# Optimization experiments

Hardware: AMD Instinct MI355X
Metric: run time of the kernel (lower is better)

## Reference

```python
import jax, jax.numpy as jnp
import numpy as np

N = 12288   # nodes
E = 393216  # edges (avg degree 32)
B = 16      # graphs in batch
F_IN = 15   # node feature dim
H = 32      # hidden_dim
EMB = 64    # embedding_dim
NC = 11     # num_classes
EDIM = 2    # edge feature dim
EPS = 1e-5  # BatchNorm eps


def _bn(x, gamma, beta):
    # training-mode BatchNorm1d: biased batch variance, matches torch normalization
    mu = jnp.mean(x, axis=0)
    var = jnp.var(x, axis=0)
    return gamma * (x - mu) * jax.lax.rsqrt(var + EPS) + beta


def setup_inputs() -> dict:
    key = jax.random.key(0)
    ks = jax.random.split(key, 16)
    def p(k, shape, s=0.05):
        return jax.random.normal(k, shape, dtype=jnp.float32) * s
    z = lambda *s: jnp.zeros(s, jnp.float32)
    o = lambda *s: jnp.ones(s, jnp.float32)
    return {
        "x": jax.random.normal(ks[0], (N, F_IN), dtype=jnp.float32),
        "edge_attr": jax.random.normal(ks[1], (E, EDIM), dtype=jnp.float32),
        "w_edge": p(ks[2], (EDIM, 1)), "b_edge": z(1),
        "w1": p(ks[3], (F_IN, H)), "b1": z(H), "g1": o(H), "be1": z(H),
        "w2": p(ks[4], (H, 2 * H)), "b2": z(2 * H), "g2": o(2 * H), "be2": z(2 * H),
        "w3": p(ks[5], (2 * H, EMB)), "b3": z(EMB), "g3": o(EMB), "be3": z(EMB),
        "wf1": p(ks[6], (EMB, 512)), "bf1": z(512), "gf1": o(512), "bef1": z(512),
        "wf2": p(ks[7], (512, 256)), "bf2": z(256), "gf2": o(256), "bef2": z(256),
        "wf3": p(ks[8], (256, NC)), "bf3": z(NC),
        "edge_index": jax.random.randint(ks[9], (2, E), 0, N, dtype=jnp.int64)
                      if jax.config.jax_enable_x64 else jax.random.randint(ks[9], (2, E), 0, N),
        "batch": jnp.sort(jax.random.randint(ks[10], (N,), 0, B)),
    }


def reference(x, edge_attr, w_edge, b_edge,
              w1, b1, g1, be1, w2, b2, g2, be2, w3, b3, g3, be3,
              wf1, bf1, gf1, bef1, wf2, bf2, gf2, bef2, wf3, bf3,
              edge_index, batch):
    # edge weights: sigmoid(Linear(edge_attr)) -> [E]
    ew = jax.nn.sigmoid(edge_attr @ w_edge + b_edge)[:, 0]
    # dense adjacency with self loops, accumulate duplicates (sparse_coo.to_dense)
    loop = jnp.arange(N)
    row = jnp.concatenate([edge_index[0], loop])
    col = jnp.concatenate([edge_index[1], loop])
    w_aug = jnp.concatenate([ew, jnp.ones((N,), ew.dtype)])
    adj = jnp.zeros((N, N), ew.dtype).at[row, col].add(w_aug)
    # symmetric degree normalization D^-1/2 A D^-1/2
    deg = adj.sum(axis=1)
    dis = jnp.where(deg > 0, jax.lax.rsqrt(jnp.where(deg > 0, deg, 1.0)), 0.0)
    support = dis[:, None] * adj * dis[None, :]
    # three GCN layers: support @ x @ W + b, BN, relu
    h = jax.nn.relu(_bn(support @ x @ w1 + b1, g1, be1))
    h = jax.nn.relu(_bn(support @ h @ w2 + b2, g2, be2))
    h = jax.nn.relu(_bn(support @ h @ w3 + b3, g3, be3))
    # global max pool per graph (empty graphs -> zeros)
    seg = jax.ops.segment_max(h, batch, num_segments=B)
    cnt = jax.ops.segment_sum(jnp.ones((N,), h.dtype), batch, num_segments=B)
    emb = jnp.where(cnt[:, None] > 0, seg, 0.0)
    # MLP head (dropout = identity at inference)
    o = jax.nn.relu(_bn(emb @ wf1 + bf1, gf1, bef1))
    o = jax.nn.relu(_bn(o @ wf2 + bf2, gf2, bef2))
    logits = o @ wf3 + bf3
    return jax.nn.log_softmax(logits, axis=1), emb
```

## Files before the change

### kernel.cpp

```cpp
#include <hip/hip_runtime.h>
#include <hip/hip_bf16.h>

#define NN   12288
#define EE   393216
#define WELL 128
#define NELL (NN*WELL)
#define BG   16
#define FIN  15
#define FH1  32
#define FH2  64
#define NCL  11
#define BNEPS 1e-5f
#define NBANK 32

typedef unsigned long long u64;
static inline int cdiv(long a, long b){ return (int)((a + b - 1) / b); }

__device__ __forceinline__ int getIdx(const void* p, long i, int is64){
  return is64 ? (int)((const long long*)p)[i] : ((const int*)p)[i];
}

__device__ __forceinline__ float degOf(u64 dc){
  return 1.0f + (float)(unsigned)(dc & 0xffffffffull) * (1.0f/1048576.0f);
}

__global__ void k_pre(u64* deg_cnt, float* csp1, float* csp2, float* csp3,
                      float* embf, const void* ei, const void* batch, int* flags){
  int g = blockIdx.x*256 + threadIdx.x;
  if (g < NN) deg_cnt[g] = 0ull;
  if (g < NBANK*128){ csp1[g] = 0.f; csp2[g] = 0.f; csp3[g] = 0.f; }
  if (g < BG*64) embf[g] = 0.f;
  if (blockIdx.x == 0 && threadIdx.x < 64){
    const int* a = (const int*)ei;
    unsigned long long m0 = __ballot(a[2*threadIdx.x + 1] == 0);
    const int* b = (const int*)batch;
    int j = 96*threadIdx.x;
    unsigned long long m1 = __ballot(b[2*j + 1] == 0);
    if (threadIdx.x == 0){
      flags[0] = (m0 == ~0ull) ? 1 : 0;
      flags[1] = (m1 == ~0ull) ? 1 : 0;
    }
  }
}

__global__ void k_edge(const float* ea, const float* we, const float* bedg,
                       const void* ei, const int* flags, u64* deg_cnt, u64* csr_p){
  int e = blockIdx.x*256 + threadIdx.x;
  if (e >= EE) return;
  int is64 = flags[0];
  float2 eav = ((const float2*)ea)[e];
  float z = eav.x*we[0] + eav.y*we[1] + bedg[0];
  float w = 1.0f/(1.0f + expf(-z));
  int r = getIdx(ei, e, is64);
  int c = getIdx(ei, (long)EE + e, is64);
  u64 add = (1ull << 32) | (u64)__float2uint_rn(w * 1048576.0f);
  u64 old = atomicAdd(&deg_cnt[r], add);
  int slot = (int)(old >> 32);
  if (slot < WELL)
    csr_p[(r << 7) + slot] = (u64)(unsigned)c | ((u64)__float_as_uint(w) << 32);
}

__global__ void k_fix(u64* csr_p, const u64* deg_cnt){
  int g = blockIdx.x*256 + threadIdx.x;
  if (g >= NELL) return;
  int row = g >> 7, s = g & (WELL-1);
  int n = (int)(deg_cnt[row] >> 32);
  n = n < WELL ? n : WELL;
  if (s >= n) return;
  u64 v = csr_p[g];
  int c = (int)(unsigned)(v & 0xffffffffull);
  float w = __uint_as_float((unsigned)(v >> 32)) * rsqrtf(degOf(deg_cnt[c]));
  ((unsigned*)csr_p)[2*g + 1] = __float_as_uint(w);
}

template<int F>
__global__ void k_stat(const float* csp, const float* g, const float* be, float* scsh){
  int f = threadIdx.x;
  if (f >= F) return;
  float s = 0.f, q = 0.f;
  #pragma unroll
  for (int b = 0; b < NBANK; b++){ s += csp[b*128 + f]; q += csp[b*128 + 64 + f]; }
  float mu  = s*(1.0f/NN);
  float var = q*(1.0f/NN) - mu*mu;
  float rinv = rsqrtf(var + BNEPS);
  float sc = g[f]*rinv;
  scsh[f]      = sc;
  scsh[64 + f] = be[f] - mu*sc;
}

template<int F, int FP, int FO, int APPLY_BN>
__global__ void __launch_bounds__(256) k_layer(
    const float* __restrict__ Hin, const float* __restrict__ scsh,
    const float* __restrict__ W, const float* __restrict__ bias,
    const u64* __restrict__ deg_cnt, const u64* __restrict__ csr_p,
    float* __restrict__ Pout, float* __restrict__ csout){
  const int R = 256/FP;
  __shared__ float At[R][FP];
  __shared__ float lcs[FO], lcq[FO];
  if (threadIdx.x < FO){ lcs[threadIdx.x] = 0.f; lcq[threadIdx.x] = 0.f; }
  int f = threadIdx.x % FP, lr = threadIdx.x / FP;
  float sc = 1.f, sh = 0.f;
  if (APPLY_BN && f < F){ sc = scsh[f]; sh = scsh[64 + f]; }
  int row = blockIdx.x*R + lr;
  if (f < F){
    u64 dc = deg_cnt[row];
    float d = rsqrtf(degOf(dc));
    int n = (int)(dc >> 32);
    n = n < WELL ? n : WELL;
    float v0 = Hin[row*F + f];
    if (APPLY_BN) v0 = fmaxf(v0*sc + sh, 0.f);
    float acc = d * v0;
    int nch = (n + 7) >> 3;
    const uint4* pb = (const uint4*)(csr_p + ((long)row << 7));
    if (nch > 0){
      uint4 a0 = pb[0], a1 = pb[1], a2 = pb[2], a3 = pb[3];
      for (int ch = 0; ch < nch; ch++){
        uint4 b0, b1, b2, b3;
        bool more = (ch + 1 < nch);
        if (more){ b0 = pb[4*ch+4]; b1 = pb[4*ch+5]; b2 = pb[4*ch+6]; b3 = pb[4*ch+7]; }
        int base = ch*8;
        if (base + 8 > n){
          if (base+0 >= n){ a0.x = 0u; a0.y = 0u; }
          if (base+1 >= n){ a0.z = 0u; a0.w = 0u; }
          if (base+2 >= n){ a1.x = 0u; a1.y = 0u; }
          if (base+3 >= n){ a1.z = 0u; a1.w = 0u; }
          if (base+4 >= n){ a2.x = 0u; a2.y = 0u; }
          if (base+5 >= n){ a2.z = 0u; a2.w = 0u; }
          if (base+6 >= n){ a3.x = 0u; a3.y = 0u; }
          if (base+7 >= n){ a3.z = 0u; a3.w = 0u; }
        }
        float h0 = Hin[(int)a0.x*F + f];
        float h1 = Hin[(int)a0.z*F + f];
        float h2 = Hin[(int)a1.x*F + f];
        float h3 = Hin[(int)a1.z*F + f];
        float h4 = Hin[(int)a2.x*F + f];
        float h5 = Hin[(int)a2.z*F + f];
        float h6 = Hin[(int)a3.x*F + f];
        float h7 = Hin[(int)a3.z*F + f];
        if (APPLY_BN){
          h0 = fmaxf(h0*sc + sh, 0.f); h1 = fmaxf(h1*sc + sh, 0.f);
          h2 = fmaxf(h2*sc + sh, 0.f); h3 = fmaxf(h3*sc + sh, 0.f);
          h4 = fmaxf(h4*sc + sh, 0.f); h5 = fmaxf(h5*sc + sh, 0.f);
          h6 = fmaxf(h6*sc + sh, 0.f); h7 = fmaxf(h7*sc + sh, 0.f);
        }
        acc += __uint_as_float(a0.y)*h0 + __uint_as_float(a0.w)*h1
             + __uint_as_float(a1.y)*h2 + __uint_as_float(a1.w)*h3
             + __uint_as_float(a2.y)*h4 + __uint_as_float(a2.w)*h5
             + __uint_as_float(a3.y)*h6 + __uint_as_float(a3.w)*h7;
        if (more){ a0 = b0; a1 = b1; a2 = b2; a3 = b3; }
      }
    }
    At[lr][f] = d * acc;
  }
  __syncthreads();
  const int fo = threadIdx.x % FO;
  float bb = bias[fo];
  for (int o = threadIdx.x; o < R*FO; o += 256){
    int l = o / FO;
    float s = bb;
    #pragma unroll
    for (int fi = 0; fi < F; fi++) s += At[l][fi] * W[fi*FO + fo];
    Pout[(blockIdx.x*R + l)*FO + fo] = s;
    atomicAdd(&lcs[fo], s);
    atomicAdd(&lcq[fo], s*s);
  }
  __syncthreads();
  if (threadIdx.x < FO){
    int bank = blockIdx.x & (NBANK-1);
    atomicAdd(&csout[bank*128 + threadIdx.x],      lcs[threadIdx.x]);
    atomicAdd(&csout[bank*128 + 64 + threadIdx.x], lcq[threadIdx.x]);
  }
}

__global__ void k_pool(const float* P3, const float* scsh, const void* batch,
                       const int* flags, float* embf){
  int is64 = flags[1];
  int b = blockIdx.x & 15, chunk = blockIdx.x >> 4;
  int lo = 0, hi = NN;
  while (lo < hi){ int m = (lo+hi)>>1; if (getIdx(batch, m, is64) < b) lo = m+1; else hi = m; }
  int start = lo;
  lo = start; hi = NN;
  while (lo < hi){ int m = (lo+hi)>>1; if (getIdx(batch, m, is64) < b+1) lo = m+1; else hi = m; }
  int end = lo;
  int f = threadIdx.x & 63, grp = threadIdx.x >> 6;
  float sc = scsh[f], sh = scsh[64 + f];
  float m = 0.0f;
  for (int i = start + chunk*4 + grp; i < end; i += 64)
    m = fmaxf(m, P3[(long)i*FH2 + f]*sc + sh);
  __shared__ float shm[4][64];
  shm[grp][f] = m;
  __syncthreads();
  if (grp == 0){
    float v = fmaxf(fmaxf(shm[0][f], shm[1][f]), fmaxf(shm[2][f], shm[3][f]));
    atomicMax((int*)&embf[b*64 + f], __float_as_int(v));
  }
}

__global__ void __launch_bounds__(256) k_fcA(const float* embf, const float* wf1,
    const float* bf1, const float* gf1, const float* bef1, float* s1g, float* out){
  if (blockIdx.x == 0){
    #pragma unroll
    for (int i = 0; i < 4; i++)
      out[BG*NCL + i*256 + threadIdx.x] = embf[i*256 + threadIdx.x];
  }
  int c = blockIdx.x*4 + (threadIdx.x >> 6);
  int l = threadIdx.x & 63;
  float wcol = wf1[l*512 + c];
  float z[BG];
  #pragma unroll
  for (int r = 0; r < BG; r++){
    float v = embf[r*64 + l] * wcol;
    #pragma unroll
    for (int off = 32; off > 0; off >>= 1) v += __shfl_down(v, off);
    z[r] = v;
  }
  if (l == 0){
    float bb = bf1[c];
    float s = 0.f, q = 0.f;
    #pragma unroll
    for (int r = 0; r < BG; r++){ float zr = z[r] + bb; s += zr; q += zr*zr; }
    float mean = s*(1.f/BG), var = q*(1.f/BG) - mean*mean;
    float inv = rsqrtf(var + BNEPS);
    float gg = gf1[c], b2 = bef1[c];
    #pragma unroll
    for (int r = 0; r < BG; r++)
      s1g[r*512 + c] = fmaxf(gg*(z[r] + bb - mean)*inv + b2, 0.f);
  }
}

__global__ void __launch_bounds__(256) k_fcB(const float* s1g, const float* wf2,
    const float* bf2, const float* gf2, const float* bef2, float* s2g){
  int c = blockIdx.x*4 + (threadIdx.x >> 6);
  int l = threadIdx.x & 63;
  float wreg[8];
  #pragma unroll
  for (int j = 0; j < 8; j++) wreg[j] = wf2[(l + 64*j)*256 + c];
  float z[BG];
  #pragma unroll
  for (int r = 0; r < BG; r++){
    float v = 0.f;
    #pragma unroll
    for (int j = 0; j < 8; j++) v += s1g[r*512 + l + 64*j] * wreg[j];
    #pragma unroll
    for (int off = 32; off > 0; off >>= 1) v += __shfl_down(v, off);
    z[r] = v;
  }
  if (l == 0){
    float bb = bf2[c];
    float s = 0.f, q = 0.f;
    #pragma unroll
    for (int r = 0; r < BG; r++){ float zr = z[r] + bb; s += zr; q += zr*zr; }
    float mean = s*(1.f/BG), var = q*(1.f/BG) - mean*mean;
    float inv = rsqrtf(var + BNEPS);
    float gg = gf2[c], b2 = bef2[c];
    #pragma unroll
    for (int r = 0; r < BG; r++)
      s2g[r*256 + c] = fmaxf(gg*(z[r] + bb - mean)*inv + b2, 0.f);
  }
}

__global__ void k_fc3(const float* s2g, const float* wf3, const float* bf3, float* out){
  __shared__ float s2[BG*256];
  __shared__ float sl[BG*NCL];
  int t = threadIdx.x;
  for (int i = t; i < BG*256; i += 256) s2[i] = s2g[i];
  __syncthreads();
  if (t < BG*NCL){
    int r = t / NCL, c = t - r*NCL;
    float s = bf3[c];
    for (int k = 0; k < 256; k++) s += s2[r*256 + k]*wf3[k*NCL + c];
    sl[t] = s;
  }
  __syncthreads();
  if (t < BG){
    float m = -1e30f;
    for (int c = 0; c < NCL; c++) m = fmaxf(m, sl[t*NCL + c]);
    float s = 0.f;
    for (int c = 0; c < NCL; c++) s += expf(sl[t*NCL + c] - m);
    float lg = logf(s) + m;
    for (int c = 0; c < NCL; c++) out[t*NCL + c] = sl[t*NCL + c] - lg;
  }
}

extern "C" void kernel_launch(void* const* d_in, const int* in_sizes, int n_in,
                              void* d_out, int out_size, void* d_ws, size_t ws_size,
                              hipStream_t stream){
  const float* x    = (const float*)d_in[0];
  const float* ea   = (const float*)d_in[1];
  const float* we   = (const float*)d_in[2];
  const float* bedg = (const float*)d_in[3];
  const float* w1   = (const float*)d_in[4];  const float* b1  = (const float*)d_in[5];
  const float* g1   = (const float*)d_in[6];  const float* be1 = (const float*)d_in[7];
  const float* w2   = (const float*)d_in[8];  const float* b2  = (const float*)d_in[9];
  const float* g2   = (const float*)d_in[10]; const float* be2 = (const float*)d_in[11];
  const float* w3   = (const float*)d_in[12]; const float* b3  = (const float*)d_in[13];
  const float* g3   = (const float*)d_in[14]; const float* be3 = (const float*)d_in[15];
  const float* wf1  = (const float*)d_in[16]; const float* bf1 = (const float*)d_in[17];
  const float* gf1  = (const float*)d_in[18]; const float* bef1= (const float*)d_in[19];
  const float* wf2  = (const float*)d_in[20]; const float* bf2 = (const float*)d_in[21];
  const float* gf2  = (const float*)d_in[22]; const float* bef2= (const float*)d_in[23];
  const float* wf3  = (const float*)d_in[24]; const float* bf3 = (const float*)d_in[25];
  const void* ei    = d_in[26];
  const void* batch = d_in[27];
  float* out = (float*)d_out;

  u64* wq = (u64*)d_ws;
  u64* deg_cnt = wq; wq += NN;
  u64* csr_p   = wq; wq += NELL;
  float* ws = (float*)wq;
  float* P1    = ws; ws += NN*FH1;
  float* P2    = ws; ws += NN*FH2;
  float* P3    = ws; ws += NN*FH2;
  float* csp1  = ws; ws += NBANK*128;
  float* csp2  = ws; ws += NBANK*128;
  float* csp3  = ws; ws += NBANK*128;
  float* scs1  = ws; ws += 128;
  float* scs2  = ws; ws += 128;
  float* scs3  = ws; ws += 128;
  float* embf  = ws; ws += BG*64;
  float* s1g   = ws; ws += BG*512;
  float* s2g   = ws; ws += BG*256;
  int* flags   = (int*)ws;

  k_pre<<<48, 256, 0, stream>>>(deg_cnt, csp1, csp2, csp3, embf, ei, batch, flags);
  k_edge<<<cdiv(EE,256), 256, 0, stream>>>(ea, we, bedg, ei, flags, deg_cnt, csr_p);
  k_fix<<<cdiv(NELL,256), 256, 0, stream>>>(csr_p, deg_cnt);

  k_layer<FIN,16,FH1,0><<<NN/16, 256, 0, stream>>>(x, nullptr,
      w1, b1, deg_cnt, csr_p, P1, csp1);
  k_stat<FH1><<<1, 64, 0, stream>>>(csp1, g1, be1, scs1);
  k_layer<FH1,32,FH2,1><<<NN/8, 256, 0, stream>>>(P1, scs1,
      w2, b2, deg_cnt, csr_p, P2, csp2);
  k_stat<FH2><<<1, 64, 0, stream>>>(csp2, g2, be2, scs2);
  k_layer<FH2,64,FH2,1><<<NN/4, 256, 0, stream>>>(P2, scs2,
      w3, b3, deg_cnt, csr_p, P3, csp3);
  k_stat<FH2><<<1, 64, 0, stream>>>(csp3, g3, be3, scs3);

  k_pool<<<256, 256, 0, stream>>>(P3, scs3, batch, flags, embf);
  k_fcA<<<128, 256, 0, stream>>>(embf, wf1, bf1, gf1, bef1, s1g, out);
  k_fcB<<<64, 256, 0, stream>>>(s1g, wf2, bf2, gf2, bef2, s2g);
  k_fc3<<<1, 256, 0, stream>>>(s2g, wf3, bf3, out);
}
```

Measured before the change: 233.6 us.

## Drop CSR fix pass, fuse BN stats into layers, merge MLP head into one kernel

Replaces the k_fix pass, which rewrote every CSR edge weight with the column's degree normalization, with a small per-node dis array that each layer gathers at aggregation time. Folds the three k_stat launches into the consumer kernels, so each block recomputes the BatchNorm scale and shift from the banked partial sums. Merges the three MLP head kernels into one 512-thread single-block kernel using shared memory. This removes a full pass over the 12M-entry padded CSR and six kernel launches, at the cost of an extra gather per edge in every layer, redundant per-block stat computation, and a serialized single-block head.

```diff
diff --git a/kernel.cpp b/kernel.cpp
--- a/kernel.cpp
+++ b/kernel.cpp
@@ -18,10 +18,6 @@
 
 __device__ __forceinline__ int getIdx(const void* p, long i, int is64){
   return is64 ? (int)((const long long*)p)[i] : ((const int*)p)[i];
-}
-
-__device__ __forceinline__ float degOf(u64 dc){
-  return 1.0f + (float)(unsigned)(dc & 0xffffffffull) * (1.0f/1048576.0f);
 }
 
 __global__ void k_pre(u64* deg_cnt, float* csp1, float* csp2, float* csp3,
@@ -57,55 +53,52 @@
   u64 old = atomicAdd(&deg_cnt[r], add);
   int slot = (int)(old >> 32);
   if (slot < WELL)
-    csr_p[(r << 7) + slot] = (u64)(unsigned)c | ((u64)__float_as_uint(w) << 32);
-}
-
-__global__ void k_fix(u64* csr_p, const u64* deg_cnt){
+    csr_p[((long)r << 7) + slot] = (u64)(unsigned)c | ((u64)__float_as_uint(w) << 32);
+}
+
+__global__ void k_dis(const u64* __restrict__ deg_cnt, float* __restrict__ dis){
   int g = blockIdx.x*256 + threadIdx.x;
-  if (g >= NELL) return;
-  int row = g >> 7, s = g & (WELL-1);
-  int n = (int)(deg_cnt[row] >> 32);
-  n = n < WELL ? n : WELL;
-  if (s >= n) return;
-  u64 v = csr_p[g];
-  int c = (int)(unsigned)(v & 0xffffffffull);
-  float w = __uint_as_float((unsigned)(v >> 32)) * rsqrtf(degOf(deg_cnt[c]));
-  ((unsigned*)csr_p)[2*g + 1] = __float_as_uint(w);
-}
-
-template<int F>
-__global__ void k_stat(const float* csp, const float* g, const float* be, float* scsh){
-  int f = threadIdx.x;
-  if (f >= F) return;
-  float s = 0.f, q = 0.f;
-  #pragma unroll
-  for (int b = 0; b < NBANK; b++){ s += csp[b*128 + f]; q += csp[b*128 + 64 + f]; }
-  float mu  = s*(1.0f/NN);
-  float var = q*(1.0f/NN) - mu*mu;
-  float rinv = rsqrtf(var + BNEPS);
-  float sc = g[f]*rinv;
-  scsh[f]      = sc;
-  scsh[64 + f] = be[f] - mu*sc;
+  if (g < NN){
+    unsigned lo = (unsigned)(deg_cnt[g] & 0xffffffffull);
+    dis[g] = rsqrtf(1.0f + (float)lo * (1.0f/1048576.0f));
+  }
 }
 
 template<int F, int FP, int FO, int APPLY_BN>
 __global__ void __launch_bounds__(256) k_layer(
-    const float* __restrict__ Hin, const float* __restrict__ scsh,
+    const float* __restrict__ Hin,
+    const float* __restrict__ cspin, const float* __restrict__ gam,
+    const float* __restrict__ bet,
     const float* __restrict__ W, const float* __restrict__ bias,
     const u64* __restrict__ deg_cnt, const u64* __restrict__ csr_p,
+    const float* __restrict__ dis,
     float* __restrict__ Pout, float* __restrict__ csout){
   const int R = 256/FP;
   __shared__ float At[R][FP];
   __shared__ float lcs[FO], lcq[FO];
+  __shared__ float lsc[64], lsh[64];
   if (threadIdx.x < FO){ lcs[threadIdx.x] = 0.f; lcq[threadIdx.x] = 0.f; }
+  if (APPLY_BN && threadIdx.x < F){
+    float s = 0.f, q = 0.f;
+    #pragma unroll
+    for (int b = 0; b < NBANK; b++){
+      s += cspin[b*128 + threadIdx.x];
+      q += cspin[b*128 + 64 + threadIdx.x];
+    }
+    float mu  = s*(1.0f/NN);
+    float var = q*(1.0f/NN) - mu*mu;
+    float sc = gam[threadIdx.x]*rsqrtf(var + BNEPS);
+    lsc[threadIdx.x] = sc;
+    lsh[threadIdx.x] = bet[threadIdx.x] - mu*sc;
+  }
+  __syncthreads();
   int f = threadIdx.x % FP, lr = threadIdx.x / FP;
   float sc = 1.f, sh = 0.f;
-  if (APPLY_BN && f < F){ sc = scsh[f]; sh = scsh[64 + f]; }
+  if (APPLY_BN && f < F){ sc = lsc[f]; sh = lsh[f]; }
   int row = blockIdx.x*R + lr;
   if (f < F){
-    u64 dc = deg_cnt[row];
-    float d = rsqrtf(degOf(dc));
-    int n = (int)(dc >> 32);
+    float d = dis[row];
+    int n = (int)(deg_cnt[row] >> 32);
     n = n < WELL ? n : WELL;
     float v0 = Hin[row*F + f];
     if (APPLY_BN) v0 = fmaxf(v0*sc + sh, 0.f);
@@ -129,6 +122,14 @@
           if (base+6 >= n){ a3.x = 0u; a3.y = 0u; }
           if (base+7 >= n){ a3.z = 0u; a3.w = 0u; }
         }
+        float w0 = __uint_as_float(a0.y) * dis[(int)a0.x];
+        float w1 = __uint_as_float(a0.w) * dis[(int)a0.z];
+        float w2 = __uint_as_float(a1.y) * dis[(int)a1.x];
+        float w3 = __uint_as_float(a1.w) * dis[(int)a1.z];
+        float w4 = __uint_as_float(a2.y) * dis[(int)a2.x];
+        float w5 = __uint_as_float(a2.w) * dis[(int)a2.z];
+        float w6 = __uint_as_float(a3.y) * dis[(int)a3.x];
+        float w7 = __uint_as_float(a3.w) * dis[(int)a3.z];
         float h0 = Hin[(int)a0.x*F + f];
         float h1 = Hin[(int)a0.z*F + f];
         float h2 = Hin[(int)a1.x*F + f];
@@ -143,10 +144,8 @@
           h4 = fmaxf(h4*sc + sh, 0.f); h5 = fmaxf(h5*sc + sh, 0.f);
           h6 = fmaxf(h6*sc + sh, 0.f); h7 = fmaxf(h7*sc + sh, 0.f);
         }
-        acc += __uint_as_float(a0.y)*h0 + __uint_as_float(a0.w)*h1
-             + __uint_as_float(a1.y)*h2 + __uint_as_float(a1.w)*h3
-             + __uint_as_float(a2.y)*h4 + __uint_as_float(a2.w)*h5
-             + __uint_as_float(a3.y)*h6 + __uint_as_float(a3.w)*h7;
+        acc += w0*h0 + w1*h1 + w2*h2 + w3*h3
+             + w4*h4 + w5*h5 + w6*h6 + w7*h7;
         if (more){ a0 = b0; a1 = b1; a2 = b2; a3 = b3; }
       }
     }
@@ -172,8 +171,24 @@
   }
 }
 
-__global__ void k_pool(const float* P3, const float* scsh, const void* batch,
-                       const int* flags, float* embf){
+__global__ void k_pool(const float* P3, const float* csp, const float* gam,
+                       const float* bet, const void* batch, const int* flags,
+                       float* embf){
+  __shared__ float lsc[64], lsh[64];
+  if (threadIdx.x < 64){
+    float s = 0.f, q = 0.f;
+    #pragma unroll
+    for (int b = 0; b < NBANK; b++){
+      s += csp[b*128 + threadIdx.x];
+      q += csp[b*128 + 64 + threadIdx.x];
+    }
+    float mu  = s*(1.0f/NN);
+    float var = q*(1.0f/NN) - mu*mu;
+    float sc = gam[threadIdx.x]*rsqrtf(var + BNEPS);
+    lsc[threadIdx.x] = sc;
+    lsh[threadIdx.x] = bet[threadIdx.x] - mu*sc;
+  }
+  __syncthreads();
   int is64 = flags[1];
   int b = blockIdx.x & 15, chunk = blockIdx.x >> 4;
   int lo = 0, hi = NN;
@@ -183,7 +198,7 @@
   while (lo < hi){ int m = (lo+hi)>>1; if (getIdx(batch, m, is64) < b+1) lo = m+1; else hi = m; }
   int end = lo;
   int f = threadIdx.x & 63, grp = threadIdx.x >> 6;
-  float sc = scsh[f], sh = scsh[64 + f];
+  float sc = lsc[f], sh = lsh[f];
   float m = 0.0f;
   for (int i = start + chunk*4 + grp; i < end; i += 64)
     m = fmaxf(m, P3[(long)i*FH2 + f]*sc + sh);
@@ -196,89 +211,117 @@
   }
 }
 
-__global__ void __launch_bounds__(256) k_fcA(const float* embf, const float* wf1,
-    const float* bf1, const float* gf1, const float* bef1, float* s1g, float* out){
-  if (blockIdx.x == 0){
-    #pragma unroll
-    for (int i = 0; i < 4; i++)
-      out[BG*NCL + i*256 + threadIdx.x] = embf[i*256 + threadIdx.x];
-  }
-  int c = blockIdx.x*4 + (threadIdx.x >> 6);
-  int l = threadIdx.x & 63;
-  float wcol = wf1[l*512 + c];
+__global__ void __launch_bounds__(512) k_head(
+    const float* __restrict__ embf,
+    const float* __restrict__ wf1, const float* __restrict__ bf1,
+    const float* __restrict__ gf1, const float* __restrict__ bef1,
+    const float* __restrict__ wf2, const float* __restrict__ bf2,
+    const float* __restrict__ gf2, const float* __restrict__ bef2,
+    const float* __restrict__ wf3, const float* __restrict__ bf3,
+    float* __restrict__ out){
+  __shared__ __align__(16) float smem[512*16 + 256*16 + 64*16];
+  float* s1T   = smem;
+  float* zp    = smem + 512*16;
+  float* sembT = smem + 512*16 + 256*16;
+  int t = threadIdx.x;
+  for (int i = t; i < BG*64; i += 512){
+    float v = embf[i];
+    out[BG*NCL + i] = v;
+    sembT[(i & 63)*16 + (i >> 6)] = v;
+  }
+  __syncthreads();
   float z[BG];
   #pragma unroll
-  for (int r = 0; r < BG; r++){
-    float v = embf[r*64 + l] * wcol;
-    #pragma unroll
-    for (int off = 32; off > 0; off >>= 1) v += __shfl_down(v, off);
-    z[r] = v;
-  }
-  if (l == 0){
-    float bb = bf1[c];
+  for (int r = 0; r < BG; r++) z[r] = 0.f;
+  #pragma unroll 4
+  for (int l = 0; l < 64; l++){
+    float w = wf1[l*512 + t];
+    const float4* e4 = (const float4*)&sembT[l*16];
+    float4 e0 = e4[0], e1 = e4[1], e2 = e4[2], e3 = e4[3];
+    z[0]  += e0.x*w; z[1]  += e0.y*w; z[2]  += e0.z*w; z[3]  += e0.w*w;
+    z[4]  += e1.x*w; z[5]  += e1.y*w; z[6]  += e1.z*w; z[7]  += e1.w*w;
+    z[8]  += e2.x*w; z[9]  += e2.y*w; z[10] += e2.z*w; z[11] += e2.w*w;
+    z[12] += e3.x*w; z[13] += e3.y*w; z[14] += e3.z*w; z[15] += e3.w*w;
+  }
+  {
+    float bb = bf1[t];
     float s = 0.f, q = 0.f;
     #pragma unroll
     for (int r = 0; r < BG; r++){ float zr = z[r] + bb; s += zr; q += zr*zr; }
-    float mean = s*(1.f/BG), var = q*(1.f/BG) - mean*mean;
+    float mean = s*(1.0f/BG), var = q*(1.0f/BG) - mean*mean;
     float inv = rsqrtf(var + BNEPS);
-    float gg = gf1[c], b2 = bef1[c];
-    #pragma unroll
-    for (int r = 0; r < BG; r++)
-      s1g[r*512 + c] = fmaxf(gg*(z[r] + bb - mean)*inv + b2, 0.f);
-  }
-}
-
-__global__ void __launch_bounds__(256) k_fcB(const float* s1g, const float* wf2,
-    const float* bf2, const float* gf2, const float* bef2, float* s2g){
-  int c = blockIdx.x*4 + (threadIdx.x >> 6);
-  int l = threadIdx.x & 63;
-  float wreg[8];
+    float gg = gf1[t], b2 = bef1[t];
+    #pragma unroll
+    for (int r = 0; r < BG; r++) z[r] = fmaxf(gg*(z[r] + bb - mean)*inv + b2, 0.f);
+    float4* s4 = (float4*)&s1T[t*16];
+    s4[0] = make_float4(z[0],  z[1],  z[2],  z[3]);
+    s4[1] = make_float4(z[4],  z[5],  z[6],  z[7]);
+    s4[2] = make_float4(z[8],  z[9],  z[10], z[11]);
+    s4[3] = make_float4(z[12], z[13], z[14], z[15]);
+  }
+  __syncthreads();
+  int c = t & 255, half = t >> 8;
+  float z2[BG];
   #pragma unroll
-  for (int j = 0; j < 8; j++) wreg[j] = wf2[(l + 64*j)*256 + c];
-  float z[BG];
-  #pragma unroll
-  for (int r = 0; r < BG; r++){
-    float v = 0.f;
-    #pragma unroll
-    for (int j = 0; j < 8; j++) v += s1g[r*512 + l + 64*j] * wreg[j];
-    #pragma unroll
-    for (int off = 32; off > 0; off >>= 1) v += __shfl_down(v, off);
-    z[r] = v;
-  }
-  if (l == 0){
+  for (int r = 0; r < BG; r++) z2[r] = 0.f;
+  int l0 = half*256;
+  #pragma unroll 2
+  for (int l = l0; l < l0 + 256; l++){
+    float w = wf2[l*256 + c];
+    const float4* e4 = (const float4*)&s1T[l*16];
+    float4 e0 = e4[0], e1 = e4[1], e2 = e4[2], e3 = e4[3];
+    z2[0]  += e0.x*w; z2[1]  += e0.y*w; z2[2]  += e0.z*w; z2[3]  += e0.w*w;
+    z2[4]  += e1.x*w; z2[5]  += e1.y*w; z2[6]  += e1.z*w; z2[7]  += e1.w*w;
+    z2[8]  += e2.x*w; z2[9]  += e2.y*w; z2[10] += e2.z*w; z2[11] += e2.w*w;
+    z2[12] += e3.x*w; z2[13] += e3.y*w; z2[14] += e3.z*w; z2[15] += e3.w*w;
+  }
+  if (half == 1){
+    float4* p4 = (float4*)&zp[c*16];
+    p4[0] = make_float4(z2[0],  z2[1],  z2[2],  z2[3]);
+    p4[1] = make_float4(z2[4],  z2[5],  z2[6],  z2[7]);
+    p4[2] = make_float4(z2[8],  z2[9],  z2[10], z2[11]);
+    p4[3] = make_float4(z2[12], z2[13], z2[14], z2[15]);
+  }
+  __syncthreads();
+  float* s2T = s1T;
+  if (half == 0){
+    const float4* p4 = (const float4*)&zp[c*16];
+    float4 q0 = p4[0], q1 = p4[1], q2 = p4[2], q3 = p4[3];
+    z2[0]  += q0.x; z2[1]  += q0.y; z2[2]  += q0.z; z2[3]  += q0.w;
+    z2[4]  += q1.x; z2[5]  += q1.y; z2[6]  += q1.z; z2[7]  += q1.w;
+    z2[8]  += q2.x; z2[9]  += q2.y; z2[10] += q2.z; z2[11] += q2.w;
+    z2[12] += q3.x; z2[13] += q3.y; z2[14] += q3.z; z2[15] += q3.w;
     float bb = bf2[c];
-    float s = 0.f, q = 0.f;
-    #pragma unroll
-    for (int r = 0; r < BG; r++){ float zr = z[r] + bb; s += zr; q += zr*zr; }
-    float mean = s*(1.f/BG), var = q*(1.f/BG) - mean*mean;
+    float s = 0.f, qq = 0.f;
+    #pragma unroll
+    for (int r = 0; r < BG; r++){ float zr = z2[r] + bb; s += zr; qq += zr*zr; }
+    float mean = s*(1.0f/BG), var = qq*(1.0f/BG) - mean*mean;
     float inv = rsqrtf(var + BNEPS);
     float gg = gf2[c], b2 = bef2[c];
     #pragma unroll
-    for (int r = 0; r < BG; r++)
-      s2g[r*256 + c] = fmaxf(gg*(z[r] + bb - mean)*inv + b2, 0.f);
-  }
-}
-
-__global__ void k_fc3(const float* s2g, const float* wf3, const float* bf3, float* out){
-  __shared__ float s2[BG*256];
-  __shared__ float sl[BG*NCL];
-  int t = threadIdx.x;
-  for (int i = t; i < BG*256; i += 256) s2[i] = s2g[i];
-  __syncthreads();
+    for (int r = 0; r < BG; r++) z2[r] = fmaxf(gg*(z2[r] + bb - mean)*inv + b2, 0.f);
+    float4* o4 = (float4*)&s2T[c*16];
+    o4[0] = make_float4(z2[0],  z2[1],  z2[2],  z2[3]);
+    o4[1] = make_float4(z2[4],  z2[5],  z2[6],  z2[7]);
+    o4[2] = make_float4(z2[8],  z2[9],  z2[10], z2[11]);
+    o4[3] = make_float4(z2[12], z2[13], z2[14], z2[15]);
+  }
+  __syncthreads();
+  float* sl = zp;
   if (t < BG*NCL){
-    int r = t / NCL, c = t - r*NCL;
-    float s = bf3[c];
-    for (int k = 0; k < 256; k++) s += s2[r*256 + k]*wf3[k*NCL + c];
-    sl[t] = s;
+    int r = t / NCL, cc = t - r*NCL;
+    float sacc = bf3[cc];
+    for (int k = 0; k < 256; k++) sacc += s2T[k*16 + r] * wf3[k*NCL + cc];
+    sl[r*16 + cc] = sacc;
   }
   __syncthreads();
   if (t < BG){
     float m = -1e30f;
-    for (int c = 0; c < NCL; c++) m = fmaxf(m, sl[t*NCL + c]);
-    float s = 0.f;
-    for (int c = 0; c < NCL; c++) s += expf(sl[t*NCL + c] - m);
-    float lg = logf(s) + m;
-    for (int c = 0; c < NCL; c++) out[t*NCL + c] = sl[t*NCL + c] - lg;
+    for (int cc = 0; cc < NCL; cc++) m = fmaxf(m, sl[t*16 + cc]);
+    float se = 0.f;
+    for (int cc = 0; cc < NCL; cc++) se += expf(sl[t*16 + cc] - m);
+    float lg = logf(se) + m;
+    for (int cc = 0; cc < NCL; cc++) out[t*NCL + cc] = sl[t*16 + cc] - lg;
   }
 }
 
@@ -314,30 +357,22 @@
   float* csp1  = ws; ws += NBANK*128;
   float* csp2  = ws; ws += NBANK*128;
   float* csp3  = ws; ws += NBANK*128;
-  float* scs1  = ws; ws += 128;
-  float* scs2  = ws; ws += 128;
-  float* scs3  = ws; ws += 128;
+  float* dis   = ws; ws += NN;
   float* embf  = ws; ws += BG*64;
-  float* s1g   = ws; ws += BG*512;
-  float* s2g   = ws; ws += BG*256;
   int* flags   = (int*)ws;
 
   k_pre<<<48, 256, 0, stream>>>(deg_cnt, csp1, csp2, csp3, embf, ei, batch, flags);
   k_edge<<<cdiv(EE,256), 256, 0, stream>>>(ea, we, bedg, ei, flags, deg_cnt, csr_p);
-  k_fix<<<cdiv(NELL,256), 256, 0, stream>>>(csr_p, deg_cnt);
-
-  k_layer<FIN,16,FH1,0><<<NN/16, 256, 0, stream>>>(x, nullptr,
-      w1, b1, deg_cnt, csr_p, P1, csp1);
-  k_stat<FH1><<<1, 64, 0, stream>>>(csp1, g1, be1, scs1);
-  k_layer<FH1,32,FH2,1><<<NN/8, 256, 0, stream>>>(P1, scs1,
-      w2, b2, deg_cnt, csr_p, P2, csp2);
-  k_stat<FH2><<<1, 64, 0, stream>>>(csp2, g2, be2, scs2);
-  k_layer<FH2,64,FH2,1><<<NN/4, 256, 0, stream>>>(P2, scs2,
-      w3, b3, deg_cnt, csr_p, P3, csp3);
-  k_stat<FH2><<<1, 64, 0, stream>>>(csp3, g3, be3, scs3);
-
-  k_pool<<<256, 256, 0, stream>>>(P3, scs3, batch, flags, embf);
-  k_fcA<<<128, 256, 0, stream>>>(embf, wf1, bf1, gf1, bef1, s1g, out);
-  k_fcB<<<64, 256, 0, stream>>>(s1g, wf2, bf2, gf2, bef2, s2g);
-  k_fc3<<<1, 256, 0, stream>>>(s2g, wf3, bf3, out);
-}
+  k_dis<<<48, 256, 0, stream>>>(deg_cnt, dis);
+
+  k_layer<FIN,16,FH1,0><<<NN/16, 256, 0, stream>>>(x, nullptr, nullptr, nullptr,
+      w1, b1, deg_cnt, csr_p, dis, P1, csp1);
+  k_layer<FH1,32,FH2,1><<<NN/8, 256, 0, stream>>>(P1, csp1, g1, be1,
+      w2, b2, deg_cnt, csr_p, dis, P2, csp2);
+  k_layer<FH2,64,FH2,1><<<NN/4, 256, 0, stream>>>(P2, csp2, g2, be2,
+      w3, b3, deg_cnt, csr_p, dis, P3, csp3);
+
+  k_pool<<<256, 256, 0, stream>>>(P3, csp3, g3, be3, batch, flags, embf);
+  k_head<<<1, 512, 0, stream>>>(embf, wf1, bf1, gf1, bef1,
+      wf2, bf2, gf2, bef2, wf3, bf3, out);
+}
```

Result: slower. 273.9 us (+17.3%).

## Replace CSR weight-fix pass with per-node dis array and fold BN stats into consumers

Applied to the files above, without the earlier changes.

Removes the k_fix kernel, which scanned the full padded ELL array (12288x128 slots) to pre-scale edge weights by the column's inverse sqrt degree. A small k_dis kernel now computes the per-node inverse sqrt degree, and the layer kernels apply it at gather time through an extra indexed load per edge. It also drops the three single-block k_stat launches by recomputing the BatchNorm scale and shift inside every block of the following layer and pool kernels. The cost is extra random reads of the dis array per edge in all three layers and redundant per-block statistic reductions.

```diff
diff --git a/kernel.cpp b/kernel.cpp
--- a/kernel.cpp
+++ b/kernel.cpp
@@ -18,10 +18,6 @@
 
 __device__ __forceinline__ int getIdx(const void* p, long i, int is64){
   return is64 ? (int)((const long long*)p)[i] : ((const int*)p)[i];
-}
-
-__device__ __forceinline__ float degOf(u64 dc){
-  return 1.0f + (float)(unsigned)(dc & 0xffffffffull) * (1.0f/1048576.0f);
 }
 
 __global__ void k_pre(u64* deg_cnt, float* csp1, float* csp2, float* csp3,
@@ -57,55 +53,52 @@
   u64 old = atomicAdd(&deg_cnt[r], add);
   int slot = (int)(old >> 32);
   if (slot < WELL)
-    csr_p[(r << 7) + slot] = (u64)(unsigned)c | ((u64)__float_as_uint(w) << 32);
-}
-
-__global__ void k_fix(u64* csr_p, const u64* deg_cnt){
+    csr_p[((long)r << 7) + slot] = (u64)(unsigned)c | ((u64)__float_as_uint(w) << 32);
+}
+
+__global__ void k_dis(const u64* __restrict__ deg_cnt, float* __restrict__ dis){
   int g = blockIdx.x*256 + threadIdx.x;
-  if (g >= NELL) return;
-  int row = g >> 7, s = g & (WELL-1);
-  int n = (int)(deg_cnt[row] >> 32);
-  n = n < WELL ? n : WELL;
-  if (s >= n) return;
-  u64 v = csr_p[g];
-  int c = (int)(unsigned)(v & 0xffffffffull);
-  float w = __uint_as_float((unsigned)(v >> 32)) * rsqrtf(degOf(deg_cnt[c]));
-  ((unsigned*)csr_p)[2*g + 1] = __float_as_uint(w);
-}
-
-template<int F>
-__global__ void k_stat(const float* csp, const float* g, const float* be, float* scsh){
-  int f = threadIdx.x;
-  if (f >= F) return;
-  float s = 0.f, q = 0.f;
-  #pragma unroll
-  for (int b = 0; b < NBANK; b++){ s += csp[b*128 + f]; q += csp[b*128 + 64 + f]; }
-  float mu  = s*(1.0f/NN);
-  float var = q*(1.0f/NN) - mu*mu;
-  float rinv = rsqrtf(var + BNEPS);
-  float sc = g[f]*rinv;
-  scsh[f]      = sc;
-  scsh[64 + f] = be[f] - mu*sc;
+  if (g < NN){
+    unsigned lo = (unsigned)(deg_cnt[g] & 0xffffffffull);
+    dis[g] = rsqrtf(1.0f + (float)lo * (1.0f/1048576.0f));
+  }
 }
 
 template<int F, int FP, int FO, int APPLY_BN>
 __global__ void __launch_bounds__(256) k_layer(
-    const float* __restrict__ Hin, const float* __restrict__ scsh,
+    const float* __restrict__ Hin,
+    const float* __restrict__ cspin, const float* __restrict__ gam,
+    const float* __restrict__ bet,
     const float* __restrict__ W, const float* __restrict__ bias,
     const u64* __restrict__ deg_cnt, const u64* __restrict__ csr_p,
+    const float* __restrict__ dis,
     float* __restrict__ Pout, float* __restrict__ csout){
   const int R = 256/FP;
   __shared__ float At[R][FP];
   __shared__ float lcs[FO], lcq[FO];
+  __shared__ float lsc[64], lsh[64];
   if (threadIdx.x < FO){ lcs[threadIdx.x] = 0.f; lcq[threadIdx.x] = 0.f; }
+  if (APPLY_BN && threadIdx.x < F){
+    float s = 0.f, q = 0.f;
+    #pragma unroll
+    for (int b = 0; b < NBANK; b++){
+      s += cspin[b*128 + threadIdx.x];
+      q += cspin[b*128 + 64 + threadIdx.x];
+    }
+    float mu  = s*(1.0f/NN);
+    float var = q*(1.0f/NN) - mu*mu;
+    float sc = gam[threadIdx.x]*rsqrtf(var + BNEPS);
+    lsc[threadIdx.x] = sc;
+    lsh[threadIdx.x] = bet[threadIdx.x] - mu*sc;
+  }
+  __syncthreads();
   int f = threadIdx.x % FP, lr = threadIdx.x / FP;
   float sc = 1.f, sh = 0.f;
-  if (APPLY_BN && f < F){ sc = scsh[f]; sh = scsh[64 + f]; }
+  if (APPLY_BN && f < F){ sc = lsc[f]; sh = lsh[f]; }
   int row = blockIdx.x*R + lr;
   if (f < F){
-    u64 dc = deg_cnt[row];
-    float d = rsqrtf(degOf(dc));
-    int n = (int)(dc >> 32);
+    float d = dis[row];
+    int n = (int)(deg_cnt[row] >> 32);
     n = n < WELL ? n : WELL;
     float v0 = Hin[row*F + f];
     if (APPLY_BN) v0 = fmaxf(v0*sc + sh, 0.f);
@@ -129,6 +122,14 @@
           if (base+6 >= n){ a3.x = 0u; a3.y = 0u; }
           if (base+7 >= n){ a3.z = 0u; a3.w = 0u; }
         }
+        float w0 = __uint_as_float(a0.y) * dis[(int)a0.x];
+        float w1 = __uint_as_float(a0.w) * dis[(int)a0.z];
+        float w2 = __uint_as_float(a1.y) * dis[(int)a1.x];
+        float w3 = __uint_as_float(a1.w) * dis[(int)a1.z];
+        float w4 = __uint_as_float(a2.y) * dis[(int)a2.x];
+        float w5 = __uint_as_float(a2.w) * dis[(int)a2.z];
+        float w6 = __uint_as_float(a3.y) * dis[(int)a3.x];
+        float w7 = __uint_as_float(a3.w) * dis[(int)a3.z];
         float h0 = Hin[(int)a0.x*F + f];
         float h1 = Hin[(int)a0.z*F + f];
         float h2 = Hin[(int)a1.x*F + f];
@@ -143,10 +144,8 @@
           h4 = fmaxf(h4*sc + sh, 0.f); h5 = fmaxf(h5*sc + sh, 0.f);
           h6 = fmaxf(h6*sc + sh, 0.f); h7 = fmaxf(h7*sc + sh, 0.f);
         }
-        acc += __uint_as_float(a0.y)*h0 + __uint_as_float(a0.w)*h1
-             + __uint_as_float(a1.y)*h2 + __uint_as_float(a1.w)*h3
-             + __uint_as_float(a2.y)*h4 + __uint_as_float(a2.w)*h5
-             + __uint_as_float(a3.y)*h6 + __uint_as_float(a3.w)*h7;
+        acc += w0*h0 + w1*h1 + w2*h2 + w3*h3
+             + w4*h4 + w5*h5 + w6*h6 + w7*h7;
         if (more){ a0 = b0; a1 = b1; a2 = b2; a3 = b3; }
       }
     }
@@ -172,8 +171,24 @@
   }
 }
 
-__global__ void k_pool(const float* P3, const float* scsh, const void* batch,
-                       const int* flags, float* embf){
+__global__ void k_pool(const float* P3, const float* csp, const float* gam,
+                       const float* bet, const void* batch, const int* flags,
+                       float* embf){
+  __shared__ float lsc[64], lsh[64];
+  if (threadIdx.x < 64){
+    float s = 0.f, q = 0.f;
+    #pragma unroll
+    for (int b = 0; b < NBANK; b++){
+      s += csp[b*128 + threadIdx.x];
+      q += csp[b*128 + 64 + threadIdx.x];
+    }
+    float mu  = s*(1.0f/NN);
+    float var = q*(1.0f/NN) - mu*mu;
+    float sc = gam[threadIdx.x]*rsqrtf(var + BNEPS);
+    lsc[threadIdx.x] = sc;
+    lsh[threadIdx.x] = bet[threadIdx.x] - mu*sc;
+  }
+  __syncthreads();
   int is64 = flags[1];
   int b = blockIdx.x & 15, chunk = blockIdx.x >> 4;
   int lo = 0, hi = NN;
@@ -183,7 +198,7 @@
   while (lo < hi){ int m = (lo+hi)>>1; if (getIdx(batch, m, is64) < b+1) lo = m+1; else hi = m; }
   int end = lo;
   int f = threadIdx.x & 63, grp = threadIdx.x >> 6;
-  float sc = scsh[f], sh = scsh[64 + f];
+  float sc = lsc[f], sh = lsh[f];
   float m = 0.0f;
   for (int i = start + chunk*4 + grp; i < end; i += 64)
     m = fmaxf(m, P3[(long)i*FH2 + f]*sc + sh);
@@ -314,9 +329,7 @@
   float* csp1  = ws; ws += NBANK*128;
   float* csp2  = ws; ws += NBANK*128;
   float* csp3  = ws; ws += NBANK*128;
-  float* scs1  = ws; ws += 128;
-  float* scs2  = ws; ws += 128;
-  float* scs3  = ws; ws += 128;
+  float* dis   = ws; ws += NN;
   float* embf  = ws; ws += BG*64;
   float* s1g   = ws; ws += BG*512;
   float* s2g   = ws; ws += BG*256;
@@ -324,19 +337,16 @@
 
   k_pre<<<48, 256, 0, stream>>>(deg_cnt, csp1, csp2, csp3, embf, ei, batch, flags);
   k_edge<<<cdiv(EE,256), 256, 0, stream>>>(ea, we, bedg, ei, flags, deg_cnt, csr_p);
-  k_fix<<<cdiv(NELL,256), 256, 0, stream>>>(csr_p, deg_cnt);
-
-  k_layer<FIN,16,FH1,0><<<NN/16, 256, 0, stream>>>(x, nullptr,
-      w1, b1, deg_cnt, csr_p, P1, csp1);
-  k_stat<FH1><<<1, 64, 0, stream>>>(csp1, g1, be1, scs1);
-  k_layer<FH1,32,FH2,1><<<NN/8, 256, 0, stream>>>(P1, scs1,
-      w2, b2, deg_cnt, csr_p, P2, csp2);
-  k_stat<FH2><<<1, 64, 0, stream>>>(csp2, g2, be2, scs2);
-  k_layer<FH2,64,FH2,1><<<NN/4, 256, 0, stream>>>(P2, scs2,
-      w3, b3, deg_cnt, csr_p, P3, csp3);
-  k_stat<FH2><<<1, 64, 0, stream>>>(csp3, g3, be3, scs3);
-
-  k_pool<<<256, 256, 0, stream>>>(P3, scs3, batch, flags, embf);
+  k_dis<<<48, 256, 0, stream>>>(deg_cnt, dis);
+
+  k_layer<FIN,16,FH1,0><<<NN/16, 256, 0, stream>>>(x, nullptr, nullptr, nullptr,
+      w1, b1, deg_cnt, csr_p, dis, P1, csp1);
+  k_layer<FH1,32,FH2,1><<<NN/8, 256, 0, stream>>>(P1, csp1, g1, be1,
+      w2, b2, deg_cnt, csr_p, dis, P2, csp2);
+  k_layer<FH2,64,FH2,1><<<NN/4, 256, 0, stream>>>(P2, csp2, g2, be2,
+      w3, b3, deg_cnt, csr_p, dis, P3, csp3);
+
+  k_pool<<<256, 256, 0, stream>>>(P3, csp3, g3, be3, batch, flags, embf);
   k_fcA<<<128, 256, 0, stream>>>(embf, wf1, bf1, gf1, bef1, s1g, out);
   k_fcB<<<64, 256, 0, stream>>>(s1g, wf2, bf2, gf2, bef2, s2g);
   k_fc3<<<1, 256, 0, stream>>>(s2g, wf3, bf3, out);
```

Measured after the change: 233.9 us. Within noise of the previous version (+0.1%).
